# Kernel tuning notes

Measured on AMD Instinct MI355X. Metric: run time of the kernel, lower is better.

The kernel has to match this reference:

```python
import jax, jax.numpy as jnp
import numpy as np


def setup_inputs() -> dict:
    key = jax.random.key(0)
    D, B, F_in, H = 8, 256, 64, 128  # depth, n_trees, n_node_features, n_hidden
    S = 2 ** D - 1                    # nodes per complete binary tree = 255
    N = B * S                         # 65280 total nodes
    # Tree structure (heap layout, root = local node 0; children of i are 2i+1, 2i+2)
    idx = np.arange(S)
    level = np.floor(np.log2(idx + 1)).astype(np.int64)      # 0 at root .. D-1 at leaves
    node_order_single = (D - 1) - level                       # leaves evaluated first (order 0)
    child_local = np.arange(1, S)
    parent_local = (child_local - 1) // 2
    offs = (np.arange(B) * S)[:, None]
    parent_g = (parent_local[None, :] + offs).reshape(-1)
    child_g = (child_local[None, :] + offs).reshape(-1)
    ks = jax.random.split(key, 8)

    def w(k, shp, fan_in):
        return (jax.random.normal(k, shp, jnp.float32) / np.sqrt(np.float32(fan_in)))

    return {
        "features": jax.random.normal(ks[0], (N, F_in), jnp.float32),
        "W_iou": w(ks[1], (F_in, 3 * H), F_in),
        "b_iou": jnp.zeros((3 * H,), jnp.float32),
        "U_iou": w(ks[2], (H, 3 * H), H),
        "W_f": w(ks[3], (F_in, H), F_in),
        "b_f": jnp.zeros((H,), jnp.float32),
        "U_f": w(ks[4], (H, H), H),
        "lin1_w": w(ks[5], (H, H), H),
        "lin1_b": jnp.zeros((H,), jnp.float32),
        "lin2_w": w(ks[6], (H, H), H),
        "lin2_b": jnp.zeros((H,), jnp.float32),
        "lin_w": w(ks[7], (H, 1), H),
        "lin_b": jnp.zeros((1,), jnp.float32),
        "node_order": jnp.asarray(np.tile(node_order_single, B), jnp.int32),
        "adjacency_list": jnp.asarray(np.stack([parent_g, child_g], axis=1), jnp.int32),
        "edge_order": jnp.asarray(np.tile(node_order_single[parent_local], B), jnp.int32),
        "n_levels": int(D),
        "n_trees": int(B),
    }


def reference(features, W_iou, b_iou, U_iou, W_f, b_f, U_f,
              lin1_w, lin1_b, lin2_w, lin2_b, lin_w, lin_b,
              node_order, adjacency_list, edge_order, n_levels, n_trees):
    N = features.shape[0]
    H = U_f.shape[0]
    parent = adjacency_list[:, 0]
    child = adjacency_list[:, 1]
    # input-to-gate projections are level-independent; compute once
    Wx_iou = features @ W_iou + b_iou   # [N, 3H]
    Wx_f = features @ W_f + b_f         # [N, H]
    h = jnp.zeros((N, H), features.dtype)
    c = jnp.zeros((N, H), features.dtype)
    for lvl in range(n_levels):  # n_levels is a static Python int
        nmask = (node_order == lvl)[:, None]
        if lvl == 0:
            iou = Wx_iou
            c_sum = jnp.zeros((N, H), features.dtype)
        else:
            emask = (edge_order == lvl)[:, None]
            child_h = jnp.where(emask, h[child], 0.0)
            h_sum = jax.ops.segment_sum(child_h, parent, num_segments=N)  # sum child h per parent
            iou = Wx_iou + h_sum @ U_iou
            f = jax.nn.sigmoid(Wx_f[parent] + h[child] @ U_f)             # per-edge forget gate
            fc = jnp.where(emask, f * c[child], 0.0)
            c_sum = jax.ops.segment_sum(fc, parent, num_segments=N)
        i, o, u = jnp.split(iou, 3, axis=1)
        c_new = jax.nn.sigmoid(i) * jnp.tanh(u) + c_sum
        h_new = jax.nn.sigmoid(o) * jnp.tanh(c_new)
        h = jnp.where(nmask, h_new, h)
        c = jnp.where(nmask, c_new, c)
    # unbatch by (equal) tree sizes and mean-pool per tree (use_root=False)
    S = N // n_trees
    x = h.reshape(n_trees, S, H).mean(axis=1)
    x = jax.nn.relu(x)                                   # dropout: identity in eval
    x = jax.nn.relu(x @ lin1_w + lin1_b)
    x = jax.nn.relu(x @ lin2_w + lin2_b)
    out = (x @ lin_w + lin_b).reshape(-1)                # torch.flatten(x)
    return out
```

## Files before the change

### kernel.cpp

```cpp
#include <hip/hip_runtime.h>
#include <hip/hip_bf16.h>
#include <math.h>

#define S_NODES 255
#define B_TREES 256
#define F_IN 64
#define H_DIM 128

typedef __attribute__((ext_vector_type(8))) short short8;
typedef __attribute__((ext_vector_type(4))) float f32x4;

__device__ __forceinline__ float fsig(float x) {
    float e = __expf(-x);
    return __builtin_amdgcn_rcpf(1.0f + e);
}
__device__ __forceinline__ float ftanh_(float x) {
    x = fminf(fmaxf(x, -15.0f), 15.0f);
    float e = __expf(2.0f * x);
    return (e - 1.0f) * __builtin_amdgcn_rcpf(e + 1.0f);
}
__device__ __forceinline__ unsigned short f2bf(float x) {
    union { __hip_bfloat16 b; unsigned short u; } v; v.b = __float2bfloat16(x); return v.u;
}
__device__ __forceinline__ float bf2f(unsigned short u) {
    union { unsigned int w; float f; } v; v.w = ((unsigned int)u) << 16; return v.f;
}
__device__ __forceinline__ unsigned int packsplit(float x) {
    unsigned short hi = f2bf(x);
    unsigned short lo = f2bf(x - bf2f(hi));
    return (unsigned)hi | ((unsigned)lo << 16);
}
__device__ __forceinline__ float unpacksplit(unsigned int u) {
    return bf2f((unsigned short)(u & 0xffffu)) + bf2f((unsigned short)(u >> 16));
}

__global__ __launch_bounds__(256) void prep_bt(
    const float* __restrict__ U_iou, const float* __restrict__ U_f,
    const float* __restrict__ W_iou, const float* __restrict__ W_f,
    unsigned short* __restrict__ Btu, unsigned short* __restrict__ Btl)
{
    int t = blockIdx.x * 256 + threadIdx.x;
    float v[8];
    char* dst;
    if (t < 512 * 24) {
        int n = t / 24, cidx = t - n * 24;
        #pragma unroll
        for (int e = 0; e < 8; ++e) {
            int k = cidx * 8 + e;
            float x;
            if (k < 128) x = (n < 384) ? U_iou[k * 384 + n] : U_f[k * 128 + (n - 384)];
            else {
                int kf = k - 128;
                x = (n < 384) ? 0.5f * W_iou[kf * 384 + n] : W_f[kf * 128 + (n - 384)];
            }
            v[e] = x;
        }
        dst = (char*)Btu + (size_t)n * 768 + cidx * 32;
    } else {
        int t2 = t - 512 * 24;
        int n = t2 >> 3, cidx = t2 & 7;
        #pragma unroll
        for (int e = 0; e < 8; ++e) v[e] = W_iou[(cidx * 8 + e) * 384 + n];
        dst = (char*)Btl + (size_t)n * 256 + cidx * 32;
    }
    unsigned int hi[4], lo[4];
    #pragma unroll
    for (int e = 0; e < 4; ++e) {
        unsigned short h0 = f2bf(v[2*e]), h1 = f2bf(v[2*e+1]);
        unsigned short s0 = f2bf(v[2*e] - bf2f(h0));
        unsigned short s1 = f2bf(v[2*e+1] - bf2f(h1));
        hi[e] = (unsigned)h0 | ((unsigned)h1 << 16);
        lo[e] = (unsigned)s0 | ((unsigned)s1 << 16);
    }
    *(uint4*)dst = make_uint4(hi[0], hi[1], hi[2], hi[3]);
    *(uint4*)(dst + 16) = make_uint4(lo[0], lo[1], lo[2], lo[3]);
}

#define MFMA(a, b, c) __builtin_amdgcn_mfma_f32_16x16x32_bf16(a, b, c, 0, 0, 0)

__global__ __launch_bounds__(512, 2) void leafgemm(
    const float* __restrict__ feat, const unsigned short* __restrict__ Btl,
    const float* __restrict__ b_iou,
    float* __restrict__ c_out, unsigned int* __restrict__ h2out)
{
    __shared__ __align__(16) char Alb[64 * 272];
    const int tid = threadIdx.x;
    const int w = tid >> 6, l = tid & 63;
    const int l15 = l & 15, l4 = l >> 4;
    const int NB = blockIdx.x << 6;

    int nct[3];
    #pragma unroll
    for (int ct = 0; ct < 3; ++ct) nct[ct] = (ct << 7) + (w << 4) + l15;

    short8 Bh[2][3], Bl[2][3];
    #define LLOADB(buf, ss) { int chb = ((ss) << 2) + l4;                           \
        _Pragma("unroll") for (int ct = 0; ct < 3; ++ct) {                          \
            const char* bp = (const char*)Btl + (size_t)nct[ct] * 256 + (chb << 5); \
            Bh[buf][ct] = *(const short8*)(bp);                                     \
            Bl[buf][ct] = *(const short8*)(bp + 16); } }

    LLOADB(0, 0)

    {
        int row = tid >> 3, o = tid & 7;
        int leafidx = NB + row;
        int tree = leafidx >> 7;
        size_t grow = (size_t)(tree * S_NODES + 127 + (leafidx & 127));
        const float* fp = feat + grow * F_IN + (o << 3);
        float4 va = *(const float4*)(fp);
        float4 vb = *(const float4*)(fp + 4);
        float vv[8] = {va.x, va.y, va.z, va.w, vb.x, vb.y, vb.z, vb.w};
        unsigned int qh[4], ql[4];
        #pragma unroll
        for (int e = 0; e < 4; ++e) {
            unsigned short h0 = f2bf(vv[2*e]), h1 = f2bf(vv[2*e+1]);
            unsigned short s0 = f2bf(vv[2*e] - bf2f(h0));
            unsigned short s1 = f2bf(vv[2*e+1] - bf2f(h1));
            qh[e] = (unsigned)h0 | ((unsigned)h1 << 16);
            ql[e] = (unsigned)s0 | ((unsigned)s1 << 16);
        }
        char* arow = Alb + row * 272;
        *(uint4*)(arow + (o << 4)) = make_uint4(qh[0], qh[1], qh[2], qh[3]);
        *(uint4*)(arow + ((8 + o) << 4)) = make_uint4(ql[0], ql[1], ql[2], ql[3]);
    }
    __syncthreads();

    f32x4 acc[4][3];
    #pragma unroll
    for (int rt = 0; rt < 4; ++rt)
        #pragma unroll
        for (int ct = 0; ct < 3; ++ct) acc[rt][ct] = (f32x4){0,0,0,0};

    #pragma unroll
    for (int s = 0; s < 2; ++s) {
        const int cur = s & 1;
        if (s < 1) LLOADB(1, 1)
        int ch = (s << 2) + l4;
        short8 ah[4], al[4];
        #pragma unroll
        for (int rt = 0; rt < 4; ++rt) {
            const char* ap = Alb + (rt * 16 + l15) * 272;
            ah[rt] = *(const short8*)(ap + (ch << 4));
            al[rt] = *(const short8*)(ap + ((8 + ch) << 4));
        }
        #pragma unroll
        for (int ct = 0; ct < 3; ++ct)
            #pragma unroll
            for (int rt = 0; rt < 4; ++rt) {
                acc[rt][ct] = MFMA(ah[rt], Bh[cur][ct], acc[rt][ct]);
                acc[rt][ct] = MFMA(al[rt], Bh[cur][ct], acc[rt][ct]);
                acc[rt][ct] = MFMA(ah[rt], Bl[cur][ct], acc[rt][ct]);
            }
    }

    const int j = (w << 4) + l15;
    float bi = b_iou[j], bo = b_iou[128 + j], bu = b_iou[256 + j];
    #pragma unroll
    for (int rt = 0; rt < 4; ++rt)
        #pragma unroll
        for (int rr = 0; rr < 4; ++rr) {
            int leafrow = rt * 16 + (l4 << 2) + rr;
            int leafidx = NB + leafrow;
            int tree = leafidx >> 7;
            size_t grow = (size_t)(tree * S_NODES + 127 + (leafidx & 127));
            float iv = acc[rt][0][rr] + bi;
            float ov = acc[rt][1][rr] + bo;
            float uv = acc[rt][2][rr] + bu;
            float cn = fsig(iv) * ftanh_(uv);
            float hn = fsig(ov) * ftanh_(cn);
            c_out[grow * 128 + j] = cn;
            h2out[grow * 128 + j] = packsplit(hn);
        }
    #undef LLOADB
}

__global__ __launch_bounds__(512, 2) void ugemm(
    const float* __restrict__ feat, const unsigned int* __restrict__ h2,
    const unsigned short* __restrict__ Btu,
    const float* __restrict__ b_iou, const float* __restrict__ b_f,
    float* __restrict__ c_io, unsigned int* __restrict__ h2out,
    int Lstart, int Lbits)
{
    __shared__ __align__(16) char Alb[64 * 784];
    const int tid = threadIdx.x;
    const int w = tid >> 6, l = tid & 63;
    const int l15 = l & 15, l4 = l >> 4;
    const int NB = blockIdx.x << 5;
    const int mask = (1 << Lbits) - 1;

    int nct[4];
    #pragma unroll
    for (int ct = 0; ct < 4; ++ct)
        nct[ct] = ((ct < 3) ? (ct << 7) : 384) + (w << 4) + l15;

    short8 Bh[2][4], Bl[2][4];
    #define ULOADB(buf, ss) { int chb = ((ss) << 2) + l4;                           \
        _Pragma("unroll") for (int ct = 0; ct < 4; ++ct) {                          \
            const char* bp = (const char*)Btu + (size_t)nct[ct] * 768 + (chb << 5); \
            Bh[buf][ct] = *(const short8*)(bp);                                     \
            Bl[buf][ct] = *(const short8*)(bp + 16); } }

    ULOADB(0, 0)

    #pragma unroll
    for (int i = 0; i < 2; ++i) {
        int tsk = tid + (i << 9);
        int row = tsk >> 4, o = tsk & 15;
        int node = NB + (row >> 1);
        int tree = node >> Lbits;
        int local = Lstart + (node & mask);
        size_t growc = (size_t)(tree * S_NODES + 2 * local + 1 + (row & 1));
        const unsigned int* hp = h2 + growc * 128 + (o << 3);
        uint4 a = *(const uint4*)(hp);
        uint4 b = *(const uint4*)(hp + 4);
        uint4 vh, vl;
        vh.x = (a.x & 0xffffu) | (a.y << 16);
        vh.y = (a.z & 0xffffu) | (a.w << 16);
        vh.z = (b.x & 0xffffu) | (b.y << 16);
        vh.w = (b.z & 0xffffu) | (b.w << 16);
        vl.x = (a.x >> 16) | (a.y & 0xffff0000u);
        vl.y = (a.z >> 16) | (a.w & 0xffff0000u);
        vl.z = (b.x >> 16) | (b.y & 0xffff0000u);
        vl.w = (b.z >> 16) | (b.w & 0xffff0000u);
        char* arow = Alb + row * 784;
        *(uint4*)(arow + (o << 4)) = vh;
        *(uint4*)(arow + ((24 + o) << 4)) = vl;
    }
    {
        int t2 = tid;
        int row = t2 >> 3, o = t2 & 7;
        int node = NB + (row >> 1);
        int tree = node >> Lbits;
        int local = Lstart + (node & mask);
        size_t growp = (size_t)(tree * S_NODES + local);
        const float* fp = feat + growp * F_IN + (o << 3);
        float4 va = *(const float4*)(fp);
        float4 vb = *(const float4*)(fp + 4);
        float vv[8] = {va.x, va.y, va.z, va.w, vb.x, vb.y, vb.z, vb.w};
        unsigned int qh[4], ql[4];
        #pragma unroll
        for (int e = 0; e < 4; ++e) {
            unsigned short h0 = f2bf(vv[2*e]), h1 = f2bf(vv[2*e+1]);
            unsigned short s0 = f2bf(vv[2*e] - bf2f(h0));
            unsigned short s1 = f2bf(vv[2*e+1] - bf2f(h1));
            qh[e] = (unsigned)h0 | ((unsigned)h1 << 16);
            ql[e] = (unsigned)s0 | ((unsigned)s1 << 16);
        }
        char* arow = Alb + row * 784;
        *(uint4*)(arow + ((16 + o) << 4)) = make_uint4(qh[0], qh[1], qh[2], qh[3]);
        *(uint4*)(arow + ((40 + o) << 4)) = make_uint4(ql[0], ql[1], ql[2], ql[3]);
    }
    __syncthreads();

    f32x4 acc[4][4];
    #pragma unroll
    for (int rt = 0; rt < 4; ++rt)
        #pragma unroll
        for (int ct = 0; ct < 4; ++ct) acc[rt][ct] = (f32x4){0,0,0,0};

    #pragma unroll
    for (int s = 0; s < 6; ++s) {
        const int cur = s & 1;
        if (s < 5) ULOADB(cur ^ 1, s + 1)
        int ch = (s << 2) + l4;
        short8 ah[4], al[4];
        #pragma unroll
        for (int rt = 0; rt < 4; ++rt) {
            const char* ap = Alb + (rt * 16 + l15) * 784;
            ah[rt] = *(const short8*)(ap + (ch << 4));
            al[rt] = *(const short8*)(ap + ((24 + ch) << 4));
        }
        #pragma unroll
        for (int ct = 0; ct < 4; ++ct)
            #pragma unroll
            for (int rt = 0; rt < 4; ++rt) {
                acc[rt][ct] = MFMA(ah[rt], Bh[cur][ct], acc[rt][ct]);
                acc[rt][ct] = MFMA(al[rt], Bh[cur][ct], acc[rt][ct]);
                acc[rt][ct] = MFMA(ah[rt], Bl[cur][ct], acc[rt][ct]);
            }
    }

    const int j = (w << 4) + l15;
    float bi = b_iou[j], bo = b_iou[128 + j], bu = b_iou[256 + j], bfv = b_f[j];
    #pragma unroll
    for (int rt = 0; rt < 4; ++rt)
        #pragma unroll
        for (int p = 0; p < 2; ++p) {
            int m = rt * 8 + (l4 << 1) + p;
            int node = NB + m;
            int tree = node >> Lbits;
            int local = Lstart + (node & mask);
            size_t gp = (size_t)(tree * S_NODES + local);
            size_t gl = (size_t)(tree * S_NODES + 2 * local + 1);
            float iv = acc[rt][0][2*p] + acc[rt][0][2*p+1] + bi;
            float ov = acc[rt][1][2*p] + acc[rt][1][2*p+1] + bo;
            float uv = acc[rt][2][2*p] + acc[rt][2][2*p+1] + bu;
            float fl = fsig(acc[rt][3][2*p] + bfv);
            float fr = fsig(acc[rt][3][2*p+1] + bfv);
            float cl = c_io[gl * 128 + j];
            float cr = c_io[(gl + 1) * 128 + j];
            float cn = fsig(iv) * ftanh_(uv) + fl * cl + fr * cr;
            float hn = fsig(ov) * ftanh_(cn);
            c_io[gp * 128 + j] = cn;
            h2out[gp * 128 + j] = packsplit(hn);
        }
    #undef ULOADB
}

__global__ __launch_bounds__(512) void readout_kernel(
    const unsigned int* __restrict__ h2,
    const float* __restrict__ lin1_w, const float* __restrict__ lin1_b,
    const float* __restrict__ lin2_w, const float* __restrict__ lin2_b,
    const float* __restrict__ lin_w, const float* __restrict__ lin_b,
    float* __restrict__ out)
{
    const int b = blockIdx.x;
    const int tid = threadIdx.x;
    const int q = tid >> 7;
    const int j = tid & 127;
    const unsigned int* hb = h2 + (size_t)b * S_NODES * H_DIM;

    float s = 0.f;
    #pragma unroll 4
    for (int n = q; n < S_NODES; n += 4) s += unpacksplit(hb[n * H_DIM + j]);

    __shared__ float part[4][H_DIM];
    __shared__ float xs[H_DIM];
    __shared__ float ys[H_DIM];
    __shared__ float red[2];

    part[q][j] = s;
    __syncthreads();
    if (tid < 128) {
        float t = (part[0][j] + part[1][j] + part[2][j] + part[3][j]) * (1.0f / 255.0f);
        xs[j] = fmaxf(t, 0.f);
    }
    __syncthreads();
    if (tid < 128) {
        float a = lin1_b[j];
        #pragma unroll 4
        for (int k = 0; k < H_DIM; ++k) a = fmaf(xs[k], lin1_w[k * H_DIM + j], a);
        ys[j] = fmaxf(a, 0.f);
    }
    __syncthreads();
    if (tid < 128) {
        float z = lin2_b[j];
        #pragma unroll 4
        for (int k = 0; k < H_DIM; ++k) z = fmaf(ys[k], lin2_w[k * H_DIM + j], z);
        z = fmaxf(z, 0.f);
        float t = z * lin_w[j];
        #pragma unroll
        for (int off = 32; off > 0; off >>= 1) t += __shfl_down(t, off, 64);
        if ((j & 63) == 0) red[j >> 6] = t;
    }
    __syncthreads();
    if (tid == 0) out[b] = red[0] + red[1] + lin_b[0];
}

extern "C" void kernel_launch(void* const* d_in, const int* in_sizes, int n_in,
                              void* d_out, int out_size, void* d_ws, size_t ws_size,
                              hipStream_t stream)
{
    const float* feat   = (const float*)d_in[0];
    const float* W_iou  = (const float*)d_in[1];
    const float* b_iou  = (const float*)d_in[2];
    const float* U_iou  = (const float*)d_in[3];
    const float* W_f    = (const float*)d_in[4];
    const float* b_f    = (const float*)d_in[5];
    const float* U_f    = (const float*)d_in[6];
    const float* lin1_w = (const float*)d_in[7];
    const float* lin1_b = (const float*)d_in[8];
    const float* lin2_w = (const float*)d_in[9];
    const float* lin2_b = (const float*)d_in[10];
    const float* lin_w  = (const float*)d_in[11];
    const float* lin_b  = (const float*)d_in[12];
    float* out = (float*)d_out;

    char* wsb = (char*)d_ws;
    unsigned short* Btu = (unsigned short*)wsb;
    unsigned short* Btl = (unsigned short*)(wsb + 393216);
    float* c  = (float*)(wsb + 524288);
    unsigned int* h2 = (unsigned int*)(wsb + 524288 + (size_t)33423360);

    prep_bt<<<60, 256, 0, stream>>>(U_iou, U_f, W_iou, W_f, Btu, Btl);

    leafgemm<<<512, 512, 0, stream>>>(feat, Btl, b_iou, c, h2);

    ugemm<<<512, 512, 0, stream>>>(feat, h2, Btu, b_iou, b_f, c, h2, 63, 6);
    ugemm<<<256, 512, 0, stream>>>(feat, h2, Btu, b_iou, b_f, c, h2, 31, 5);
    ugemm<<<128, 512, 0, stream>>>(feat, h2, Btu, b_iou, b_f, c, h2, 15, 4);
    ugemm<<<64,  512, 0, stream>>>(feat, h2, Btu, b_iou, b_f, c, h2,  7, 3);
    ugemm<<<32,  512, 0, stream>>>(feat, h2, Btu, b_iou, b_f, c, h2,  3, 2);
    ugemm<<<16,  512, 0, stream>>>(feat, h2, Btu, b_iou, b_f, c, h2,  1, 1);
    ugemm<<<8,   512, 0, stream>>>(feat, h2, Btu, b_iou, b_f, c, h2,  0, 0);

    readout_kernel<<<B_TREES, 512, 0, stream>>>(
        h2, lin1_w, lin1_b, lin2_w, lin2_b, lin_w, lin_b, out);
}
```

Before: 271.7 us.

## Fuse top four tree levels into one per-tree kernel with LDS state

Replaces the four separate ugemm launches for the top tree levels (7,3,1,0 nodes per tree) with a single toptile kernel, one block per tree. Each block loads level-4 h/c into shared memory and runs the remaining levels in a loop with split-bf16 MFMA, keeping h and c in LDS between levels. This aims to cut launch overhead and the poor occupancy of tiny grids (8–64 blocks), at the cost of mostly idle MFMA rows on the small top levels.

```diff
diff --git a/kernel.cpp b/kernel.cpp
--- a/kernel.cpp
+++ b/kernel.cpp
@@ -308,6 +308,134 @@
     #undef ULOADB
 }
 
+__global__ __launch_bounds__(512, 2) void toptile(
+    const float* __restrict__ feat, const unsigned int* __restrict__ h2g,
+    const float* __restrict__ c_g, const unsigned short* __restrict__ Btu,
+    const float* __restrict__ b_iou, const float* __restrict__ b_f,
+    unsigned int* __restrict__ h2out)
+{
+    __shared__ unsigned int h2s[31][H_DIM];
+    __shared__ float cs[31][H_DIM];
+    __shared__ __align__(16) char Alb[16 * 784];
+    const int tid = threadIdx.x;
+    const int w = tid >> 6, l = tid & 63;
+    const int l15 = l & 15, l4 = l >> 4;
+    const size_t tb = (size_t)blockIdx.x * S_NODES;
+
+    {
+        int row = tid >> 5, c4 = (tid & 31) << 2;
+        *(uint4*)&h2s[15 + row][c4] = *(const uint4*)(h2g + (tb + 15 + row) * H_DIM + c4);
+        *(float4*)&cs[15 + row][c4] = *(const float4*)(c_g + (tb + 15 + row) * H_DIM + c4);
+    }
+    __syncthreads();
+
+    int nct[4];
+    #pragma unroll
+    for (int ct = 0; ct < 4; ++ct)
+        nct[ct] = ((ct < 3) ? (ct << 7) : 384) + (w << 4) + l15;
+
+    const int j = (w << 4) + l15;
+    const float bi = b_iou[j], bo = b_iou[128 + j], bu = b_iou[256 + j], bfv = b_f[j];
+
+    const int bases[4] = {7, 3, 1, 0};
+    const int cnts[4]  = {8, 4, 2, 1};
+
+    for (int lev = 0; lev < 4; ++lev) {
+        const int base = bases[lev], cnt = cnts[lev];
+        const int rows = cnt << 1;
+
+        if (tid < rows * 16) {
+            int r = tid >> 4, o = tid & 15;
+            int child = 2 * (base + (r >> 1)) + 1 + (r & 1);
+            const unsigned int* hp = &h2s[child][o << 3];
+            unsigned int u0 = hp[0], u1 = hp[1], u2 = hp[2], u3 = hp[3];
+            unsigned int u4 = hp[4], u5 = hp[5], u6 = hp[6], u7 = hp[7];
+            uint4 vh, vl;
+            vh.x = (u0 & 0xffffu) | (u1 << 16);
+            vh.y = (u2 & 0xffffu) | (u3 << 16);
+            vh.z = (u4 & 0xffffu) | (u5 << 16);
+            vh.w = (u6 & 0xffffu) | (u7 << 16);
+            vl.x = (u0 >> 16) | (u1 & 0xffff0000u);
+            vl.y = (u2 >> 16) | (u3 & 0xffff0000u);
+            vl.z = (u4 >> 16) | (u5 & 0xffff0000u);
+            vl.w = (u6 >> 16) | (u7 & 0xffff0000u);
+            char* arow = Alb + r * 784;
+            *(uint4*)(arow + (o << 4)) = vh;
+            *(uint4*)(arow + ((24 + o) << 4)) = vl;
+        } else if (tid < rows * 24) {
+            int t2 = tid - rows * 16;
+            int r = t2 >> 3, o = t2 & 7;
+            int parent = base + (r >> 1);
+            const float* fp = feat + (tb + parent) * F_IN + (o << 3);
+            float4 va = *(const float4*)(fp);
+            float4 vb = *(const float4*)(fp + 4);
+            float vv[8] = {va.x, va.y, va.z, va.w, vb.x, vb.y, vb.z, vb.w};
+            unsigned int qh[4], ql[4];
+            #pragma unroll
+            for (int e = 0; e < 4; ++e) {
+                unsigned short h0 = f2bf(vv[2*e]), h1 = f2bf(vv[2*e+1]);
+                unsigned short s0 = f2bf(vv[2*e] - bf2f(h0));
+                unsigned short s1 = f2bf(vv[2*e+1] - bf2f(h1));
+                qh[e] = (unsigned)h0 | ((unsigned)h1 << 16);
+                ql[e] = (unsigned)s0 | ((unsigned)s1 << 16);
+            }
+            char* arow = Alb + r * 784;
+            *(uint4*)(arow + ((16 + o) << 4)) = make_uint4(qh[0], qh[1], qh[2], qh[3]);
+            *(uint4*)(arow + ((40 + o) << 4)) = make_uint4(ql[0], ql[1], ql[2], ql[3]);
+        }
+        __syncthreads();
+
+        f32x4 acc[4];
+        #pragma unroll
+        for (int ct = 0; ct < 4; ++ct) acc[ct] = (f32x4){0,0,0,0};
+        short8 Bh[2][4], Bl[2][4];
+        #define TLOADB(buf, ss) { int chb = ((ss) << 2) + l4;                           \
+            _Pragma("unroll") for (int ct = 0; ct < 4; ++ct) {                          \
+                const char* bp = (const char*)Btu + (size_t)nct[ct] * 768 + (chb << 5); \
+                Bh[buf][ct] = *(const short8*)(bp);                                     \
+                Bl[buf][ct] = *(const short8*)(bp + 16); } }
+        TLOADB(0, 0)
+        #pragma unroll
+        for (int s = 0; s < 6; ++s) {
+            const int cur = s & 1;
+            if (s < 5) TLOADB(cur ^ 1, s + 1)
+            int ch = (s << 2) + l4;
+            const char* ap = Alb + l15 * 784;
+            short8 ah = *(const short8*)(ap + (ch << 4));
+            short8 al = *(const short8*)(ap + ((24 + ch) << 4));
+            #pragma unroll
+            for (int ct = 0; ct < 4; ++ct) {
+                acc[ct] = MFMA(ah, Bh[cur][ct], acc[ct]);
+                acc[ct] = MFMA(al, Bh[cur][ct], acc[ct]);
+                acc[ct] = MFMA(ah, Bl[cur][ct], acc[ct]);
+            }
+        }
+        #undef TLOADB
+
+        #pragma unroll
+        for (int p = 0; p < 2; ++p) {
+            int m = (l4 << 1) + p;
+            if (m < cnt) {
+                int local = base + m;
+                float iv = acc[0][2*p] + acc[0][2*p+1] + bi;
+                float ov = acc[1][2*p] + acc[1][2*p+1] + bo;
+                float uv = acc[2][2*p] + acc[2][2*p+1] + bu;
+                float fl = fsig(acc[3][2*p] + bfv);
+                float fr = fsig(acc[3][2*p+1] + bfv);
+                float cl = cs[2*local+1][j];
+                float cr = cs[2*local+2][j];
+                float cn = fsig(iv) * ftanh_(uv) + fl * cl + fr * cr;
+                float hn = fsig(ov) * ftanh_(cn);
+                cs[local][j] = cn;
+                unsigned int pk = packsplit(hn);
+                h2s[local][j] = pk;
+                h2out[(tb + local) * H_DIM + j] = pk;
+            }
+        }
+        __syncthreads();
+    }
+}
+
 __global__ __launch_bounds__(512) void readout_kernel(
     const unsigned int* __restrict__ h2,
     const float* __restrict__ lin1_w, const float* __restrict__ lin1_b,
@@ -390,10 +518,8 @@
     ugemm<<<512, 512, 0, stream>>>(feat, h2, Btu, b_iou, b_f, c, h2, 63, 6);
     ugemm<<<256, 512, 0, stream>>>(feat, h2, Btu, b_iou, b_f, c, h2, 31, 5);
     ugemm<<<128, 512, 0, stream>>>(feat, h2, Btu, b_iou, b_f, c, h2, 15, 4);
-    ugemm<<<64,  512, 0, stream>>>(feat, h2, Btu, b_iou, b_f, c, h2,  7, 3);
-    ugemm<<<32,  512, 0, stream>>>(feat, h2, Btu, b_iou, b_f, c, h2,  3, 2);
-    ugemm<<<16,  512, 0, stream>>>(feat, h2, Btu, b_iou, b_f, c, h2,  1, 1);
-    ugemm<<<8,   512, 0, stream>>>(feat, h2, Btu, b_iou, b_f, c, h2,  0, 0);
+
+    toptile<<<B_TREES, 512, 0, stream>>>(feat, h2, c, Btu, b_iou, b_f, h2);
 
     readout_kernel<<<B_TREES, 512, 0, stream>>>(
         h2, lin1_w, lin1_b, lin2_w, lin2_b, lin_w, lin_b, out);
```

Result: faster. 227.7 us (-16.2%).

## Fuse upper tree levels and readout into one per-tree kernel

Applied to the files above, without the earlier changes.

Replaces six small per-level ugemm launches (levels 5..0) and the separate readout kernel with a single kernel that runs one block per tree. Each block processes levels 31..0 of its own tree in sequence with block-level barriers, then mean-pools and applies the MLP head. This removes launch overhead and the low-occupancy tail grids of the upper levels. The cost is that upper-level MFMA tiles are mostly padding, and all work sits in 256 blocks that run serially through six dependent levels.

```diff
diff --git a/kernel.cpp b/kernel.cpp
--- a/kernel.cpp
+++ b/kernel.cpp
@@ -174,6 +174,7 @@
         }
     #undef LLOADB
 }
+
 
 __global__ __launch_bounds__(512, 2) void ugemm(
     const float* __restrict__ feat, const unsigned int* __restrict__ h2,
@@ -308,54 +309,186 @@
     #undef ULOADB
 }
 
-__global__ __launch_bounds__(512) void readout_kernel(
-    const unsigned int* __restrict__ h2,
+__global__ __launch_bounds__(512, 2) void deeptop(
+    const float* __restrict__ feat, const unsigned int* __restrict__ h2,
+    const unsigned short* __restrict__ Btu,
+    const float* __restrict__ b_iou, const float* __restrict__ b_f,
+    float* __restrict__ c_io, unsigned int* __restrict__ h2out,
     const float* __restrict__ lin1_w, const float* __restrict__ lin1_b,
     const float* __restrict__ lin2_w, const float* __restrict__ lin2_b,
     const float* __restrict__ lin_w, const float* __restrict__ lin_b,
     float* __restrict__ out)
 {
-    const int b = blockIdx.x;
-    const int tid = threadIdx.x;
-    const int q = tid >> 7;
-    const int j = tid & 127;
-    const unsigned int* hb = h2 + (size_t)b * S_NODES * H_DIM;
-
-    float s = 0.f;
-    #pragma unroll 4
-    for (int n = q; n < S_NODES; n += 4) s += unpacksplit(hb[n * H_DIM + j]);
-
+    __shared__ __align__(16) char Alb[64 * 784];
     __shared__ float part[4][H_DIM];
     __shared__ float xs[H_DIM];
     __shared__ float ys[H_DIM];
     __shared__ float red[2];
 
-    part[q][j] = s;
-    __syncthreads();
-    if (tid < 128) {
-        float t = (part[0][j] + part[1][j] + part[2][j] + part[3][j]) * (1.0f / 255.0f);
-        xs[j] = fmaxf(t, 0.f);
-    }
-    __syncthreads();
-    if (tid < 128) {
-        float a = lin1_b[j];
+    const int tid = threadIdx.x;
+    const int w = tid >> 6, l = tid & 63;
+    const int l15 = l & 15, l4 = l >> 4;
+    const size_t tb = (size_t)blockIdx.x * S_NODES;
+
+    int nct[4];
+    #pragma unroll
+    for (int ct = 0; ct < 4; ++ct)
+        nct[ct] = ((ct < 3) ? (ct << 7) : 384) + (w << 4) + l15;
+    const int j = (w << 4) + l15;
+    const float bi = b_iou[j], bo = b_iou[128 + j], bu = b_iou[256 + j], bfv = b_f[j];
+
+    #define DLOADB(buf, ss) { int chb = ((ss) << 2) + l4;                           \
+        _Pragma("unroll") for (int ct = 0; ct < 4; ++ct) {                          \
+            const char* bp = (const char*)Btu + (size_t)nct[ct] * 768 + (chb << 5); \
+            Bh[buf][ct] = *(const short8*)(bp);                                     \
+            Bl[buf][ct] = *(const short8*)(bp + 16); } }
+
+    #define LEVEL_PASS(NRT, base, cnt)                                              \
+    {                                                                               \
+        const int rows = (cnt) << 1;                                                \
+        _Pragma("unroll")                                                           \
+        for (int i = 0; i < 3; ++i) {                                               \
+            int tsk = tid + (i << 9);                                               \
+            if (tsk < rows * 16) {                                                  \
+                int row = tsk >> 4, o = tsk & 15;                                   \
+                int m = row >> 1;                                                   \
+                int local = (base) + m;                                             \
+                size_t growc = tb + 2 * local + 1 + (row & 1);                      \
+                const unsigned int* hp = h2 + growc * 128 + (o << 3);               \
+                uint4 a = *(const uint4*)(hp);                                      \
+                uint4 b = *(const uint4*)(hp + 4);                                  \
+                uint4 vh, vl;                                                       \
+                vh.x = (a.x & 0xffffu) | (a.y << 16);                               \
+                vh.y = (a.z & 0xffffu) | (a.w << 16);                               \
+                vh.z = (b.x & 0xffffu) | (b.y << 16);                               \
+                vh.w = (b.z & 0xffffu) | (b.w << 16);                               \
+                vl.x = (a.x >> 16) | (a.y & 0xffff0000u);                           \
+                vl.y = (a.z >> 16) | (a.w & 0xffff0000u);                           \
+                vl.z = (b.x >> 16) | (b.y & 0xffff0000u);                           \
+                vl.w = (b.z >> 16) | (b.w & 0xffff0000u);                           \
+                char* arow = Alb + row * 784;                                       \
+                *(uint4*)(arow + (o << 4)) = vh;                                    \
+                *(uint4*)(arow + ((24 + o) << 4)) = vl;                             \
+            } else if (tsk < rows * 24) {                                           \
+                int t2 = tsk - rows * 16;                                           \
+                int row = t2 >> 3, o = t2 & 7;                                      \
+                int local = (base) + (row >> 1);                                    \
+                const float* fp = feat + (tb + local) * F_IN + (o << 3);            \
+                float4 va = *(const float4*)(fp);                                   \
+                float4 vb = *(const float4*)(fp + 4);                               \
+                float vv[8] = {va.x, va.y, va.z, va.w, vb.x, vb.y, vb.z, vb.w};     \
+                unsigned int qh[4], ql[4];                                          \
+                _Pragma("unroll")                                                   \
+                for (int e = 0; e < 4; ++e) {                                       \
+                    unsigned short h0 = f2bf(vv[2*e]), h1 = f2bf(vv[2*e+1]);        \
+                    unsigned short s0 = f2bf(vv[2*e] - bf2f(h0));                   \
+                    unsigned short s1 = f2bf(vv[2*e+1] - bf2f(h1));                 \
+                    qh[e] = (unsigned)h0 | ((unsigned)h1 << 16);                    \
+                    ql[e] = (unsigned)s0 | ((unsigned)s1 << 16);                    \
+                }                                                                   \
+                char* arow = Alb + row * 784;                                       \
+                *(uint4*)(arow + ((16 + o) << 4)) = make_uint4(qh[0], qh[1], qh[2], qh[3]); \
+                *(uint4*)(arow + ((40 + o) << 4)) = make_uint4(ql[0], ql[1], ql[2], ql[3]); \
+            }                                                                       \
+        }                                                                           \
+        __syncthreads();                                                            \
+        f32x4 acc[NRT][4];                                                          \
+        _Pragma("unroll")                                                           \
+        for (int rt = 0; rt < NRT; ++rt)                                            \
+            _Pragma("unroll")                                                       \
+            for (int ct = 0; ct < 4; ++ct) acc[rt][ct] = (f32x4){0,0,0,0};          \
+        short8 Bh[2][4], Bl[2][4];                                                  \
+        DLOADB(0, 0)                                                                \
+        _Pragma("unroll")                                                           \
+        for (int s = 0; s < 6; ++s) {                                               \
+            const int cur = s & 1;                                                  \
+            if (s < 5) DLOADB(cur ^ 1, s + 1)                                       \
+            int ch = (s << 2) + l4;                                                 \
+            short8 ah[NRT], al[NRT];                                                \
+            _Pragma("unroll")                                                       \
+            for (int rt = 0; rt < NRT; ++rt) {                                      \
+                const char* ap = Alb + (rt * 16 + l15) * 784;                       \
+                ah[rt] = *(const short8*)(ap + (ch << 4));                          \
+                al[rt] = *(const short8*)(ap + ((24 + ch) << 4));                   \
+            }                                                                       \
+            _Pragma("unroll")                                                       \
+            for (int ct = 0; ct < 4; ++ct)                                          \
+                _Pragma("unroll")                                                   \
+                for (int rt = 0; rt < NRT; ++rt) {                                  \
+                    acc[rt][ct] = MFMA(ah[rt], Bh[cur][ct], acc[rt][ct]);           \
+                    acc[rt][ct] = MFMA(al[rt], Bh[cur][ct], acc[rt][ct]);           \
+                    acc[rt][ct] = MFMA(ah[rt], Bl[cur][ct], acc[rt][ct]);           \
+                }                                                                   \
+        }                                                                           \
+        _Pragma("unroll")                                                           \
+        for (int rt = 0; rt < NRT; ++rt)                                            \
+            _Pragma("unroll")                                                       \
+            for (int p = 0; p < 2; ++p) {                                           \
+                int m = rt * 8 + (l4 << 1) + p;                                     \
+                if (m < (cnt)) {                                                    \
+                    int local = (base) + m;                                         \
+                    size_t gp = tb + local;                                         \
+                    size_t gl = tb + 2 * local + 1;                                 \
+                    float iv = acc[rt][0][2*p] + acc[rt][0][2*p+1] + bi;            \
+                    float ov = acc[rt][1][2*p] + acc[rt][1][2*p+1] + bo;            \
+                    float uv = acc[rt][2][2*p] + acc[rt][2][2*p+1] + bu;            \
+                    float fl = fsig(acc[rt][3][2*p] + bfv);                         \
+                    float fr = fsig(acc[rt][3][2*p+1] + bfv);                       \
+                    float cl = c_io[gl * 128 + j];                                  \
+                    float cr = c_io[(gl + 1) * 128 + j];                            \
+                    float cn = fsig(iv) * ftanh_(uv) + fl * cl + fr * cr;           \
+                    float hn = fsig(ov) * ftanh_(cn);                               \
+                    c_io[gp * 128 + j] = cn;                                        \
+                    h2out[gp * 128 + j] = packsplit(hn);                            \
+                }                                                                   \
+            }                                                                       \
+        __syncthreads();                                                            \
+    }
+
+    LEVEL_PASS(4, 31, 32)
+    LEVEL_PASS(2, 15, 16)
+    LEVEL_PASS(1, 7, 8)
+    LEVEL_PASS(1, 3, 4)
+    LEVEL_PASS(1, 1, 2)
+    LEVEL_PASS(1, 0, 1)
+    #undef LEVEL_PASS
+    #undef DLOADB
+
+    {
+        const int q = tid >> 7;
+        const int jr = tid & 127;
+        const unsigned int* hb = h2 + tb * H_DIM;
+
+        float s = 0.f;
         #pragma unroll 4
-        for (int k = 0; k < H_DIM; ++k) a = fmaf(xs[k], lin1_w[k * H_DIM + j], a);
-        ys[j] = fmaxf(a, 0.f);
-    }
-    __syncthreads();
-    if (tid < 128) {
-        float z = lin2_b[j];
-        #pragma unroll 4
-        for (int k = 0; k < H_DIM; ++k) z = fmaf(ys[k], lin2_w[k * H_DIM + j], z);
-        z = fmaxf(z, 0.f);
-        float t = z * lin_w[j];
-        #pragma unroll
-        for (int off = 32; off > 0; off >>= 1) t += __shfl_down(t, off, 64);
-        if ((j & 63) == 0) red[j >> 6] = t;
-    }
-    __syncthreads();
-    if (tid == 0) out[b] = red[0] + red[1] + lin_b[0];
+        for (int n = q; n < S_NODES; n += 4) s += unpacksplit(hb[n * H_DIM + jr]);
+        part[q][jr] = s;
+        __syncthreads();
+        if (tid < 128) {
+            float t = (part[0][jr] + part[1][jr] + part[2][jr] + part[3][jr]) * (1.0f / 255.0f);
+            xs[jr] = fmaxf(t, 0.f);
+        }
+        __syncthreads();
+        if (tid < 128) {
+            float a = lin1_b[jr];
+            #pragma unroll 4
+            for (int k = 0; k < H_DIM; ++k) a = fmaf(xs[k], lin1_w[k * H_DIM + jr], a);
+            ys[jr] = fmaxf(a, 0.f);
+        }
+        __syncthreads();
+        if (tid < 128) {
+            float z = lin2_b[jr];
+            #pragma unroll 4
+            for (int k = 0; k < H_DIM; ++k) z = fmaf(ys[k], lin2_w[k * H_DIM + jr], z);
+            z = fmaxf(z, 0.f);
+            float t = z * lin_w[jr];
+            #pragma unroll
+            for (int off = 32; off > 0; off >>= 1) t += __shfl_down(t, off, 64);
+            if ((jr & 63) == 0) red[jr >> 6] = t;
+        }
+        __syncthreads();
+        if (tid == 0) out[blockIdx.x] = red[0] + red[1] + lin_b[0];
+    }
 }
 
 extern "C" void kernel_launch(void* const* d_in, const int* in_sizes, int n_in,
@@ -388,13 +521,8 @@
     leafgemm<<<512, 512, 0, stream>>>(feat, Btl, b_iou, c, h2);
 
     ugemm<<<512, 512, 0, stream>>>(feat, h2, Btu, b_iou, b_f, c, h2, 63, 6);
-    ugemm<<<256, 512, 0, stream>>>(feat, h2, Btu, b_iou, b_f, c, h2, 31, 5);
-    ugemm<<<128, 512, 0, stream>>>(feat, h2, Btu, b_iou, b_f, c, h2, 15, 4);
-    ugemm<<<64,  512, 0, stream>>>(feat, h2, Btu, b_iou, b_f, c, h2,  7, 3);
-    ugemm<<<32,  512, 0, stream>>>(feat, h2, Btu, b_iou, b_f, c, h2,  3, 2);
-    ugemm<<<16,  512, 0, stream>>>(feat, h2, Btu, b_iou, b_f, c, h2,  1, 1);
-    ugemm<<<8,   512, 0, stream>>>(feat, h2, Btu, b_iou, b_f, c, h2,  0, 0);
-
-    readout_kernel<<<B_TREES, 512, 0, stream>>>(
-        h2, lin1_w, lin1_b, lin2_w, lin2_b, lin_w, lin_b, out);
-}
+
+    deeptop<<<B_TREES, 512, 0, stream>>>(feat, h2, Btu, b_iou, b_f, c, h2,
+                                         lin1_w, lin1_b, lin2_w, lin2_b,
+                                         lin_w, lin_b, out);
+}
```

Result: faster. 239.9 us (-11.7%).
